# Optimization experiments

Hardware: AMD Instinct MI355X
Metric: run time of the kernel (lower is better)

The kernel has to match this reference:

```python
import jax, jax.numpy as jnp
import numpy as np

B, S, H = 2, 1024, 2048
E, K, I = 32, 4, 512   # num_experts, top_k, moe_intermediate
IS = 512               # shared_expert_intermediate


def setup_inputs() -> dict:
    key = jax.random.key(0)
    ks = jax.random.split(key, 10)
    s = 0.02
    return {
        "hidden_states": jax.random.normal(ks[0], (B, S, H), jnp.float32),
        "Wr": jax.random.normal(ks[1], (E, H), jnp.float32) * s,      # router gate
        "Wg": jax.random.normal(ks[2], (E, I, H), jnp.float32) * s,   # expert gate_proj
        "Wu": jax.random.normal(ks[3], (E, I, H), jnp.float32) * s,   # expert up_proj
        "Wd": jax.random.normal(ks[4], (E, H, I), jnp.float32) * s,   # expert down_proj
        "Wsg": jax.random.normal(ks[5], (IS, H), jnp.float32) * s,    # shared gate_proj
        "Wsu": jax.random.normal(ks[6], (IS, H), jnp.float32) * s,    # shared up_proj
        "Wsd": jax.random.normal(ks[7], (H, IS), jnp.float32) * s,    # shared down_proj
        "Wsgate": jax.random.normal(ks[8], (1, H), jnp.float32) * s,  # shared_expert_gate
    }


def reference(hidden_states, Wr, Wg, Wu, Wd, Wsg, Wsu, Wsd, Wsgate):
    b, s, h = hidden_states.shape
    x = hidden_states.reshape(-1, h)                      # [T, H]
    T = x.shape[0]

    # router: softmax in fp32, top-k, renormalize (norm_topk_prob=True)
    router_logits = x @ Wr.T                               # [T, E]
    rw = jax.nn.softmax(router_logits.astype(jnp.float32), axis=-1)
    vals, idx = jax.lax.top_k(rw, K)                       # [T, K]
    vals = vals / jnp.sum(vals, axis=-1, keepdims=True)
    vals = vals.astype(x.dtype)

    # combine-weight matrix: zeros except selected experts
    C = jnp.zeros((T, E), x.dtype).at[jnp.arange(T)[:, None], idx].add(vals)

    # all experts evaluate all tokens (calibrate_all_experts path); combine zeros non-selected
    g = jnp.einsum('th,eih->tei', x, Wg)                   # [T, E, I]
    u = jnp.einsum('th,eih->tei', x, Wu)
    hact = jax.nn.silu(g) * u
    moe_out = jnp.einsum('tei,ehi,te->th', hact, Wd, C)    # weighted combine

    # shared expert with sigmoid gate
    shared = (jax.nn.silu(x @ Wsg.T) * (x @ Wsu.T)) @ Wsd.T
    gate = jax.nn.sigmoid(x @ Wsgate.T)                    # [T, 1]
    out = (moe_out + gate * shared).reshape(b, s, h)
    return out, router_logits
```

## Files before the change

kernel.cpp:

```cpp
#include <hip/hip_runtime.h>
#include <math.h>

#define T_N 2048
#define H_N 2048
#define E_N 32
#define I_N 512
#define NA_MOE (T_N*4)
#define NA_ALL (NA_MOE + T_N)
#define BM 128
#define BK 32
#define MAXT 112

typedef short s16x8 __attribute__((ext_vector_type(8)));
typedef float f32x4 __attribute__((ext_vector_type(4)));

__device__ inline short f2bf(float f){
    unsigned int u = __float_as_uint(f);
    u = (u + 0x7fffu + ((u >> 16) & 1u)) >> 16;
    return (short)u;
}
__device__ inline float bf2f(short s){
    return __uint_as_float(((unsigned int)(unsigned short)s) << 16);
}
__device__ inline s16x8 cvt8(float4 f0, float4 f1){
    s16x8 v;
    v[0]=f2bf(f0.x); v[1]=f2bf(f0.y); v[2]=f2bf(f0.z); v[3]=f2bf(f0.w);
    v[4]=f2bf(f1.x); v[5]=f2bf(f1.y); v[6]=f2bf(f1.z); v[7]=f2bf(f1.w);
    return v;
}

__global__ __launch_bounds__(256) void cast_x_kernel(const float* __restrict__ x,
                                                     short* __restrict__ xbf){
    size_t i = (size_t)(blockIdx.x * 256 + threadIdx.x) * 8;
    float4 a = *(const float4*)(x + i);
    float4 b = *(const float4*)(x + i + 4);
    *(s16x8*)(xbf + i) = cvt8(a, b);
}

__global__ __launch_bounds__(64) void router_kernel(
    const float* __restrict__ x, const float* __restrict__ Wr,
    const float* __restrict__ Wsgate,
    float* __restrict__ logits_out, int* __restrict__ tidx, float* __restrict__ tw,
    int* __restrict__ perm, float* __restrict__ wgt, int* __restrict__ counts)
{
    const int t = blockIdx.x, lane = threadIdx.x;
    const float* xr = x + (size_t)t * H_N;
    float xv[32];
    #pragma unroll
    for (int i = 0; i < 32; i++) xv[i] = xr[i*64 + lane];
    __shared__ float lg[34];
    for (int e = 0; e < 33; e++){
        const float* wr = (e < 32) ? (Wr + (size_t)e * H_N) : Wsgate;
        double s = 0.0;
        #pragma unroll
        for (int i = 0; i < 32; i++) s += (double)xv[i] * (double)wr[i*64 + lane];
        #pragma unroll
        for (int o = 32; o > 0; o >>= 1) s += __shfl_down(s, o);
        if (lane == 0) lg[e] = (float)s;
    }
    __syncthreads();
    if (lane < 32) logits_out[(size_t)t*32 + lane] = lg[lane];
    if (lane == 0){
        float m = lg[0];
        for (int e = 1; e < 32; e++) m = fmaxf(m, lg[e]);
        unsigned mask = 0; int sel[4]; float sv[4]; float s4 = 0.f;
        for (int k = 0; k < 4; k++){
            int best = -1; float bv = -1e30f;
            for (int e = 0; e < 32; e++)
                if (!((mask >> e) & 1u) && lg[e] > bv){ bv = lg[e]; best = e; }
            mask |= 1u << best; sel[k] = best;
            float p = expf(lg[best] - m); sv[k] = p; s4 += p;
        }
        for (int k = 0; k < 4; k++){
            tidx[t*4 + k] = sel[k];
            tw[t*4 + k]   = sv[k] / s4;
            atomicAdd(&counts[sel[k]], 1);
        }
        perm[NA_MOE + t] = t;
        wgt[NA_MOE + t]  = 1.f / (1.f + expf(-lg[32]));
    }
}

__global__ void scan_kernel(int* ctrl){
    if (threadIdx.x == 0){
        int* counts = ctrl; int* eoff = ctrl + 128; int* ecnt = ctrl + 192;
        int acc = 0;
        for (int e = 0; e < 32; e++){ eoff[e] = acc; ecnt[e] = counts[e]; acc += counts[e]; }
        eoff[32] = NA_MOE; ecnt[32] = T_N;
        int nt = 0;
        for (int e = 0; e < 33; e++){
            int c = ecnt[e];
            for (int m = 0; m * BM < c; m++) ctrl[260 + nt++] = (e << 16) | m;
        }
        ctrl[256] = nt;
    }
    if (threadIdx.x < 64) ctrl[64 + threadIdx.x] = 0;
}

__global__ __launch_bounds__(256) void scatter_kernel(
    const int* __restrict__ tidx, const float* __restrict__ tw,
    int* __restrict__ perm, float* __restrict__ wgt, int* __restrict__ apos,
    int* ctrl)
{
    int t = blockIdx.x * 256 + threadIdx.x;
    if (t >= T_N) return;
    const int* eoff = ctrl + 128; int* cursor = ctrl + 64;
    for (int k = 0; k < 4; k++){
        int e = tidx[t*4 + k];
        int pos = eoff[e] + atomicAdd(&cursor[e], 1);
        perm[pos] = t; wgt[pos] = tw[t*4 + k]; apos[t*4 + k] = pos;
    }
}

__global__ __launch_bounds__(256, 3) void gemm1_kernel(
    const short* __restrict__ xbf,
    const float* __restrict__ Wg, const float* __restrict__ Wu,
    const float* __restrict__ Wsg, const float* __restrict__ Wsu,
    const int* __restrict__ perm, const int* __restrict__ ctrl,
    short* __restrict__ hact)
{
    const int tile = blockIdx.x >> 3;
    if (tile >= ctrl[256]) return;
    const int wrk = ctrl[260 + tile];
    const int e   = wrk >> 16;
    const int m0  = (wrk & 0xffff) << 7;
    const int cnt = ctrl[192 + e];
    const int off = ctrl[128 + e];
    const int n0  = (blockIdx.x & 7) << 6;

    __shared__ s16x8 lsA[2][4*128];
    __shared__ s16x8 lsBg[2][4*64];
    __shared__ s16x8 lsBu[2][4*64];

    const int tid = threadIdx.x;
    const int r_a = tid & 127;
    const int kca = tid >> 7;
    const short* arow = nullptr;
    if (m0 + r_a < cnt) arow = xbf + (size_t)perm[off + m0 + r_a] * H_N;

    const int rb = tid >> 2, kcb = tid & 3;
    const float *browg, *browu;
    if (e < 32){
        browg = Wg + ((size_t)e * I_N + (n0 + rb)) * H_N + kcb*8;
        browu = Wu + ((size_t)e * I_N + (n0 + rb)) * H_N + kcb*8;
    } else {
        browg = Wsg + (size_t)(n0 + rb) * H_N + kcb*8;
        browu = Wsu + (size_t)(n0 + rb) * H_N + kcb*8;
    }

    const int wid = tid >> 6, lane = tid & 63;
    const int wm = wid >> 1, wn = wid & 1;
    const int kg = lane >> 4, l15 = lane & 15;

    f32x4 accg[4][2], accu[4][2];
    #pragma unroll
    for (int a = 0; a < 4; a++)
        #pragma unroll
        for (int b = 0; b < 2; b++)
            #pragma unroll
            for (int j = 0; j < 4; j++){ accg[a][b][j] = 0.f; accu[a][b][j] = 0.f; }

    {
        s16x8 a0{}, a1{};
        if (arow){
            a0 = *(const s16x8*)(arow + kca*8);
            a1 = *(const s16x8*)(arow + (kca+2)*8);
        }
        lsA[0][kca*128 + r_a]     = a0;
        lsA[0][(kca+2)*128 + r_a] = a1;
        float4 g0 = *(const float4*)(browg);
        float4 g1 = *(const float4*)(browg + 4);
        float4 u0 = *(const float4*)(browu);
        float4 u1 = *(const float4*)(browu + 4);
        lsBg[0][kcb*64 + rb] = cvt8(g0, g1);
        lsBu[0][kcb*64 + rb] = cvt8(u0, u1);
    }
    s16x8 pa0{}, pa1{};
    if (arow){
        pa0 = *(const s16x8*)(arow + BK + kca*8);
        pa1 = *(const s16x8*)(arow + BK + (kca+2)*8);
    }
    float4 pg0 = *(const float4*)(browg + BK);
    float4 pg1 = *(const float4*)(browg + BK + 4);
    float4 pu0 = *(const float4*)(browu + BK);
    float4 pu1 = *(const float4*)(browu + BK + 4);

    int cur = 0;
    for (int k0 = 0; k0 < H_N; k0 += BK){
        __syncthreads();
        s16x8 na0{}, na1{};
        float4 ng0{}, ng1{}, nu0{}, nu1{};
        if (k0 + 2*BK < H_N){
            const int kn = k0 + 2*BK;
            if (arow){
                na0 = *(const s16x8*)(arow + kn + kca*8);
                na1 = *(const s16x8*)(arow + kn + (kca+2)*8);
            }
            ng0 = *(const float4*)(browg + kn);
            ng1 = *(const float4*)(browg + kn + 4);
            nu0 = *(const float4*)(browu + kn);
            nu1 = *(const float4*)(browu + kn + 4);
        }
        if (k0 + BK < H_N){
            const int nb = cur ^ 1;
            lsA[nb][kca*128 + r_a]     = pa0;
            lsA[nb][(kca+2)*128 + r_a] = pa1;
            lsBg[nb][kcb*64 + rb] = cvt8(pg0, pg1);
            lsBu[nb][kcb*64 + rb] = cvt8(pu0, pu1);
        }
        #pragma unroll
        for (int mf = 0; mf < 4; mf++){
            s16x8 a = lsA[cur][kg*128 + wm*64 + mf*16 + l15];
            #pragma unroll
            for (int nf = 0; nf < 2; nf++){
                s16x8 bg = lsBg[cur][kg*64 + wn*32 + nf*16 + l15];
                s16x8 bu = lsBu[cur][kg*64 + wn*32 + nf*16 + l15];
                accg[mf][nf] = __builtin_amdgcn_mfma_f32_16x16x32_bf16(a, bg, accg[mf][nf], 0, 0, 0);
                accu[mf][nf] = __builtin_amdgcn_mfma_f32_16x16x32_bf16(a, bu, accu[mf][nf], 0, 0, 0);
            }
        }
        pa0 = na0; pa1 = na1;
        pg0 = ng0; pg1 = ng1; pu0 = nu0; pu1 = nu1;
        cur ^= 1;
    }
    #pragma unroll
    for (int mf = 0; mf < 4; mf++){
        #pragma unroll
        for (int j = 0; j < 4; j++){
            int row = m0 + wm*64 + mf*16 + kg*4 + j;
            if (row < cnt){
                #pragma unroll
                for (int nf = 0; nf < 2; nf++){
                    int col = n0 + wn*32 + nf*16 + l15;
                    float g = accg[mf][nf][j], u = accu[mf][nf][j];
                    float h = g / (1.f + expf(-g)) * u;
                    hact[(size_t)(off + row) * I_N + col] = f2bf(h);
                }
            }
        }
    }
}

template<int USE_Y>
__global__ __launch_bounds__(256, 3) void gemm2_kernel(
    const short* __restrict__ hact,
    const float* __restrict__ Wd, const float* __restrict__ Wsd,
    const int* __restrict__ perm, const float* __restrict__ wgt,
    const int* __restrict__ ctrl, float* __restrict__ out, short* __restrict__ y)
{
    const int tile = blockIdx.x >> 5;
    if (tile >= ctrl[256]) return;
    const int wrk = ctrl[260 + tile];
    const int e   = wrk >> 16;
    const int m0  = (wrk & 0xffff) << 7;
    const int cnt = ctrl[192 + e];
    const int off = ctrl[128 + e];
    const int n0  = (blockIdx.x & 31) << 6;

    __shared__ s16x8 lsA[2][4*128];
    __shared__ s16x8 lsB[2][4*64];

    const int tid = threadIdx.x;
    const int r_a = tid & 127;
    const int kca = tid >> 7;
    const short* arow = nullptr;
    if (m0 + r_a < cnt) arow = hact + (size_t)(off + m0 + r_a) * I_N;

    const int rb = tid >> 2, kcb = tid & 3;
    const float* brow = (e < 32) ? (Wd  + ((size_t)e * H_N + (n0 + rb)) * I_N + kcb*8)
                                 : (Wsd + (size_t)(n0 + rb) * I_N + kcb*8);

    const int wid = tid >> 6, lane = tid & 63;
    const int wm = wid >> 1, wn = wid & 1;
    const int kg = lane >> 4, l15 = lane & 15;

    f32x4 acc[4][2];
    #pragma unroll
    for (int a = 0; a < 4; a++)
        #pragma unroll
        for (int b = 0; b < 2; b++)
            #pragma unroll
            for (int j = 0; j < 4; j++) acc[a][b][j] = 0.f;

    {
        s16x8 a0{}, a1{};
        if (arow){
            a0 = *(const s16x8*)(arow + kca*8);
            a1 = *(const s16x8*)(arow + (kca+2)*8);
        }
        lsA[0][kca*128 + r_a]     = a0;
        lsA[0][(kca+2)*128 + r_a] = a1;
        float4 f0 = *(const float4*)(brow);
        float4 f1 = *(const float4*)(brow + 4);
        lsB[0][kcb*64 + rb] = cvt8(f0, f1);
    }
    s16x8 pa0{}, pa1{};
    if (arow){
        pa0 = *(const s16x8*)(arow + BK + kca*8);
        pa1 = *(const s16x8*)(arow + BK + (kca+2)*8);
    }
    float4 pf0 = *(const float4*)(brow + BK);
    float4 pf1 = *(const float4*)(brow + BK + 4);

    int cur = 0;
    for (int k0 = 0; k0 < I_N; k0 += BK){
        __syncthreads();
        s16x8 na0{}, na1{};
        float4 nf0{}, nf1{};
        if (k0 + 2*BK < I_N){
            const int kn = k0 + 2*BK;
            if (arow){
                na0 = *(const s16x8*)(arow + kn + kca*8);
                na1 = *(const s16x8*)(arow + kn + (kca+2)*8);
            }
            nf0 = *(const float4*)(brow + kn);
            nf1 = *(const float4*)(brow + kn + 4);
        }
        if (k0 + BK < I_N){
            const int nb = cur ^ 1;
            lsA[nb][kca*128 + r_a]     = pa0;
            lsA[nb][(kca+2)*128 + r_a] = pa1;
            lsB[nb][kcb*64 + rb] = cvt8(pf0, pf1);
        }
        #pragma unroll
        for (int mf = 0; mf < 4; mf++){
            s16x8 a = lsA[cur][kg*128 + wm*64 + mf*16 + l15];
            #pragma unroll
            for (int nf = 0; nf < 2; nf++){
                s16x8 b = lsB[cur][kg*64 + wn*32 + nf*16 + l15];
                acc[mf][nf] = __builtin_amdgcn_mfma_f32_16x16x32_bf16(a, b, acc[mf][nf], 0, 0, 0);
            }
        }
        pa0 = na0; pa1 = na1; pf0 = nf0; pf1 = nf1;
        cur ^= 1;
    }
    #pragma unroll
    for (int mf = 0; mf < 4; mf++){
        #pragma unroll
        for (int j = 0; j < 4; j++){
            int row = m0 + wm*64 + mf*16 + kg*4 + j;
            if (row < cnt){
                int aidx = off + row;
                if (USE_Y){
                    #pragma unroll
                    for (int nf = 0; nf < 2; nf++){
                        int col = n0 + wn*32 + nf*16 + l15;
                        y[(size_t)aidx * H_N + col] = f2bf(acc[mf][nf][j]);
                    }
                } else {
                    int tok = perm[aidx];
                    float w = wgt[aidx];
                    #pragma unroll
                    for (int nf = 0; nf < 2; nf++){
                        int col = n0 + wn*32 + nf*16 + l15;
                        atomicAdd(&out[(size_t)tok * H_N + col], w * acc[mf][nf][j]);
                    }
                }
            }
        }
    }
}

__global__ __launch_bounds__(256) void combine_kernel(
    const short* __restrict__ y, const int* __restrict__ apos,
    const float* __restrict__ tw, const float* __restrict__ wgt,
    float* __restrict__ out)
{
    const int t = blockIdx.x;
    const int c0 = threadIdx.x * 8;
    float acc[8];
    {
        float ws = wgt[NA_MOE + t];
        s16x8 v = *(const s16x8*)(y + (size_t)(NA_MOE + t) * H_N + c0);
        #pragma unroll
        for (int j = 0; j < 8; j++) acc[j] = ws * bf2f(v[j]);
    }
    #pragma unroll
    for (int k = 0; k < 4; k++){
        int p   = apos[t*4 + k];
        float w = tw[t*4 + k];
        s16x8 v = *(const s16x8*)(y + (size_t)p * H_N + c0);
        #pragma unroll
        for (int j = 0; j < 8; j++) acc[j] += w * bf2f(v[j]);
    }
    float4 o0 = make_float4(acc[0], acc[1], acc[2], acc[3]);
    float4 o1 = make_float4(acc[4], acc[5], acc[6], acc[7]);
    *(float4*)(out + (size_t)t * H_N + c0)     = o0;
    *(float4*)(out + (size_t)t * H_N + c0 + 4) = o1;
}

extern "C" void kernel_launch(void* const* d_in, const int* in_sizes, int n_in,
                              void* d_out, int out_size, void* d_ws, size_t ws_size,
                              hipStream_t stream)
{
    const float* x      = (const float*)d_in[0];
    const float* Wr     = (const float*)d_in[1];
    const float* Wg     = (const float*)d_in[2];
    const float* Wu     = (const float*)d_in[3];
    const float* Wd     = (const float*)d_in[4];
    const float* Wsg    = (const float*)d_in[5];
    const float* Wsu    = (const float*)d_in[6];
    const float* Wsd    = (const float*)d_in[7];
    const float* Wsgate = (const float*)d_in[8];

    float* out    = (float*)d_out;
    float* logits = out + (size_t)T_N * H_N;

    char* ws = (char*)d_ws;
    short* xbf  = (short*)ws;
    short* hact = (short*)(ws + 8388608);
    int*   perm = (int*)(ws + 18874368);
    float* wgt  = (float*)(ws + 18915328);
    int*   tidx = (int*)(ws + 18956288);
    float* tw   = (float*)(ws + 18989056);
    int*   apos = (int*)(ws + 19021824);
    int*   ctrl = (int*)(ws + 19054592);
    short* y    = (short*)(ws + 19056640);
    const size_t Y_END = 19056640ull + 41943040ull;
    const bool use_y = (ws_size >= Y_END);

    hipMemsetAsync(ctrl, 0, 256 * sizeof(int), stream);
    if (!use_y)
        hipMemsetAsync(d_out, 0, (size_t)T_N * H_N * sizeof(float), stream);

    cast_x_kernel<<<2048, 256, 0, stream>>>(x, xbf);
    router_kernel<<<T_N, 64, 0, stream>>>(x, Wr, Wsgate, logits, tidx, tw, perm, wgt, ctrl);
    scan_kernel<<<1, 64, 0, stream>>>(ctrl);
    scatter_kernel<<<T_N/256, 256, 0, stream>>>(tidx, tw, perm, wgt, apos, ctrl);
    gemm1_kernel<<<MAXT*8, 256, 0, stream>>>(xbf, Wg, Wu, Wsg, Wsu, perm, ctrl, hact);
    if (use_y){
        gemm2_kernel<1><<<MAXT*32, 256, 0, stream>>>(hact, Wd, Wsd, perm, wgt, ctrl, out, y);
        combine_kernel<<<T_N, 256, 0, stream>>>(y, apos, tw, wgt, out);
    } else {
        gemm2_kernel<0><<<MAXT*32, 256, 0, stream>>>(hact, Wd, Wsd, perm, wgt, ctrl, out, y);
    }
}
```

Baseline: 366.6 us.

## Use 256-row tiles, split-K gemm1 with fixup kernel, reorder shared tiles first

Raises the M tile to 256 rows in both grouped GEMMs, so each expert weight tile is reused across more tokens and fewer fp32 weight reads plus bf16 conversions are needed. To keep enough blocks in flight for gemm1, it narrows N to 32 and can split the H reduction in two. The split writes fp32 partials for gate and up, and a new fixup kernel sums them and applies SiLU. The shared-expert tiles are now scheduled first. The split path costs about 80MB of extra partial-sum traffic and one more launch, and only runs when the workspace is large enough.

```diff
diff --git a/kernel.cpp b/kernel.cpp
--- a/kernel.cpp
+++ b/kernel.cpp
@@ -7,9 +7,10 @@
 #define I_N 512
 #define NA_MOE (T_N*4)
 #define NA_ALL (NA_MOE + T_N)
-#define BM 128
+#define BM 256
 #define BK 32
-#define MAXT 112
+#define MAXT 72
+#define PART_FLOATS 10485760ull
 
 typedef short s16x8 __attribute__((ext_vector_type(8)));
 typedef float f32x4 __attribute__((ext_vector_type(4)));
@@ -88,7 +89,8 @@
         for (int e = 0; e < 32; e++){ eoff[e] = acc; ecnt[e] = counts[e]; acc += counts[e]; }
         eoff[32] = NA_MOE; ecnt[32] = T_N;
         int nt = 0;
-        for (int e = 0; e < 33; e++){
+        for (int m = 0; m * BM < T_N; m++) ctrl[260 + nt++] = (32 << 16) | m;
+        for (int e = 0; e < 32; e++){
             int c = ecnt[e];
             for (int m = 0; m * BM < c; m++) ctrl[260 + nt++] = (e << 16) | m;
         }
@@ -112,44 +114,43 @@
     }
 }
 
+template<int KS>
 __global__ __launch_bounds__(256, 3) void gemm1_kernel(
     const short* __restrict__ xbf,
     const float* __restrict__ Wg, const float* __restrict__ Wu,
     const float* __restrict__ Wsg, const float* __restrict__ Wsu,
     const int* __restrict__ perm, const int* __restrict__ ctrl,
-    short* __restrict__ hact)
-{
-    const int tile = blockIdx.x >> 3;
+    short* __restrict__ hact, float* __restrict__ part)
+{
+    const int bid  = blockIdx.x;
+    const int tile = bid / (16*KS);
     if (tile >= ctrl[256]) return;
+    const int sub = bid % (16*KS);
+    const int nb  = (KS==2) ? (sub >> 1) : sub;
+    const int kh  = (KS==2) ? (sub & 1) : 0;
+    const int KH  = H_N / KS;
     const int wrk = ctrl[260 + tile];
     const int e   = wrk >> 16;
-    const int m0  = (wrk & 0xffff) << 7;
+    const int m0  = (wrk & 0xffff) << 8;
     const int cnt = ctrl[192 + e];
     const int off = ctrl[128 + e];
-    const int n0  = (blockIdx.x & 7) << 6;
-
-    __shared__ s16x8 lsA[2][4*128];
-    __shared__ s16x8 lsBg[2][4*64];
-    __shared__ s16x8 lsBu[2][4*64];
+    const int n0  = nb * 32;
+
+    __shared__ s16x8 lsA[2][4*256];
+    __shared__ s16x8 lsBg[2][4*32];
+    __shared__ s16x8 lsBu[2][4*32];
 
     const int tid = threadIdx.x;
-    const int r_a = tid & 127;
-    const int kca = tid >> 7;
     const short* arow = nullptr;
-    if (m0 + r_a < cnt) arow = xbf + (size_t)perm[off + m0 + r_a] * H_N;
-
-    const int rb = tid >> 2, kcb = tid & 3;
-    const float *browg, *browu;
-    if (e < 32){
-        browg = Wg + ((size_t)e * I_N + (n0 + rb)) * H_N + kcb*8;
-        browu = Wu + ((size_t)e * I_N + (n0 + rb)) * H_N + kcb*8;
-    } else {
-        browg = Wsg + (size_t)(n0 + rb) * H_N + kcb*8;
-        browu = Wsu + (size_t)(n0 + rb) * H_N + kcb*8;
-    }
+    if (m0 + tid < cnt) arow = xbf + (size_t)perm[off + m0 + tid] * H_N + kh*KH;
+    const int tb  = tid & 127;
+    const int rb  = tb & 31, kcb = tb >> 5;
+    const float* brow;
+    if (e < 32) brow = ((tid < 128) ? Wg : Wu) + ((size_t)e*I_N + n0 + rb)*H_N + kh*KH + kcb*8;
+    else        brow = ((tid < 128) ? Wsg : Wsu) + (size_t)(n0 + rb)*H_N + kh*KH + kcb*8;
 
     const int wid = tid >> 6, lane = tid & 63;
-    const int wm = wid >> 1, wn = wid & 1;
+    const int wm = wid;
     const int kg = lane >> 4, l15 = lane & 15;
 
     f32x4 accg[4][2], accu[4][2];
@@ -161,84 +162,130 @@
             for (int j = 0; j < 4; j++){ accg[a][b][j] = 0.f; accu[a][b][j] = 0.f; }
 
     {
-        s16x8 a0{}, a1{};
+        s16x8 a[4] = {{0},{0},{0},{0}};
         if (arow){
-            a0 = *(const s16x8*)(arow + kca*8);
-            a1 = *(const s16x8*)(arow + (kca+2)*8);
-        }
-        lsA[0][kca*128 + r_a]     = a0;
-        lsA[0][(kca+2)*128 + r_a] = a1;
-        float4 g0 = *(const float4*)(browg);
-        float4 g1 = *(const float4*)(browg + 4);
-        float4 u0 = *(const float4*)(browu);
-        float4 u1 = *(const float4*)(browu + 4);
-        lsBg[0][kcb*64 + rb] = cvt8(g0, g1);
-        lsBu[0][kcb*64 + rb] = cvt8(u0, u1);
-    }
-    s16x8 pa0{}, pa1{};
+            #pragma unroll
+            for (int kc = 0; kc < 4; kc++) a[kc] = *(const s16x8*)(arow + kc*8);
+        }
+        #pragma unroll
+        for (int kc = 0; kc < 4; kc++) lsA[0][kc*256 + tid] = a[kc];
+        float4 f0 = *(const float4*)(brow);
+        float4 f1 = *(const float4*)(brow + 4);
+        ((tid < 128) ? lsBg[0] : lsBu[0])[kcb*32 + rb] = cvt8(f0, f1);
+    }
+    s16x8 pa[4] = {{0},{0},{0},{0}};
     if (arow){
-        pa0 = *(const s16x8*)(arow + BK + kca*8);
-        pa1 = *(const s16x8*)(arow + BK + (kca+2)*8);
-    }
-    float4 pg0 = *(const float4*)(browg + BK);
-    float4 pg1 = *(const float4*)(browg + BK + 4);
-    float4 pu0 = *(const float4*)(browu + BK);
-    float4 pu1 = *(const float4*)(browu + BK + 4);
+        #pragma unroll
+        for (int kc = 0; kc < 4; kc++) pa[kc] = *(const s16x8*)(arow + BK + kc*8);
+    }
+    float4 pf0 = *(const float4*)(brow + BK);
+    float4 pf1 = *(const float4*)(brow + BK + 4);
 
     int cur = 0;
-    for (int k0 = 0; k0 < H_N; k0 += BK){
+    for (int k0 = 0; k0 < KH; k0 += BK){
         __syncthreads();
-        s16x8 na0{}, na1{};
-        float4 ng0{}, ng1{}, nu0{}, nu1{};
-        if (k0 + 2*BK < H_N){
+        s16x8 na[4] = {{0},{0},{0},{0}};
+        float4 nf0{}, nf1{};
+        if (k0 + 2*BK < KH){
             const int kn = k0 + 2*BK;
             if (arow){
-                na0 = *(const s16x8*)(arow + kn + kca*8);
-                na1 = *(const s16x8*)(arow + kn + (kca+2)*8);
-            }
-            ng0 = *(const float4*)(browg + kn);
-            ng1 = *(const float4*)(browg + kn + 4);
-            nu0 = *(const float4*)(browu + kn);
-            nu1 = *(const float4*)(browu + kn + 4);
-        }
-        if (k0 + BK < H_N){
-            const int nb = cur ^ 1;
-            lsA[nb][kca*128 + r_a]     = pa0;
-            lsA[nb][(kca+2)*128 + r_a] = pa1;
-            lsBg[nb][kcb*64 + rb] = cvt8(pg0, pg1);
-            lsBu[nb][kcb*64 + rb] = cvt8(pu0, pu1);
+                #pragma unroll
+                for (int kc = 0; kc < 4; kc++) na[kc] = *(const s16x8*)(arow + kn + kc*8);
+            }
+            nf0 = *(const float4*)(brow + kn);
+            nf1 = *(const float4*)(brow + kn + 4);
+        }
+        if (k0 + BK < KH){
+            const int nbuf = cur ^ 1;
+            #pragma unroll
+            for (int kc = 0; kc < 4; kc++) lsA[nbuf][kc*256 + tid] = pa[kc];
+            ((tid < 128) ? lsBg[nbuf] : lsBu[nbuf])[kcb*32 + rb] = cvt8(pf0, pf1);
         }
         #pragma unroll
         for (int mf = 0; mf < 4; mf++){
-            s16x8 a = lsA[cur][kg*128 + wm*64 + mf*16 + l15];
+            s16x8 a = lsA[cur][kg*256 + wm*64 + mf*16 + l15];
             #pragma unroll
             for (int nf = 0; nf < 2; nf++){
-                s16x8 bg = lsBg[cur][kg*64 + wn*32 + nf*16 + l15];
-                s16x8 bu = lsBu[cur][kg*64 + wn*32 + nf*16 + l15];
+                s16x8 bg = lsBg[cur][kg*32 + nf*16 + l15];
+                s16x8 bu = lsBu[cur][kg*32 + nf*16 + l15];
                 accg[mf][nf] = __builtin_amdgcn_mfma_f32_16x16x32_bf16(a, bg, accg[mf][nf], 0, 0, 0);
                 accu[mf][nf] = __builtin_amdgcn_mfma_f32_16x16x32_bf16(a, bu, accu[mf][nf], 0, 0, 0);
             }
         }
-        pa0 = na0; pa1 = na1;
-        pg0 = ng0; pg1 = ng1; pu0 = nu0; pu1 = nu1;
+        #pragma unroll
+        for (int kc = 0; kc < 4; kc++) pa[kc] = na[kc];
+        pf0 = nf0; pf1 = nf1;
         cur ^= 1;
     }
-    #pragma unroll
-    for (int mf = 0; mf < 4; mf++){
-        #pragma unroll
-        for (int j = 0; j < 4; j++){
-            int row = m0 + wm*64 + mf*16 + kg*4 + j;
-            if (row < cnt){
-                #pragma unroll
-                for (int nf = 0; nf < 2; nf++){
-                    int col = n0 + wn*32 + nf*16 + l15;
-                    float g = accg[mf][nf][j], u = accu[mf][nf][j];
-                    float h = g / (1.f + expf(-g)) * u;
-                    hact[(size_t)(off + row) * I_N + col] = f2bf(h);
+
+    if (KS == 2){
+        float* pb = part + (size_t)kh * PART_FLOATS;
+        #pragma unroll
+        for (int mf = 0; mf < 4; mf++){
+            #pragma unroll
+            for (int j = 0; j < 4; j++){
+                int row = m0 + wm*64 + mf*16 + kg*4 + j;
+                if (row < cnt){
+                    float* pr = pb + (size_t)(off + row) * 1024 + n0;
+                    #pragma unroll
+                    for (int nf = 0; nf < 2; nf++){
+                        __builtin_nontemporal_store(accg[mf][nf][j], pr + nf*16 + l15);
+                        __builtin_nontemporal_store(accu[mf][nf][j], pr + 512 + nf*16 + l15);
+                    }
                 }
             }
         }
-    }
+    } else {
+        #pragma unroll
+        for (int mf = 0; mf < 4; mf++){
+            #pragma unroll
+            for (int j = 0; j < 4; j++){
+                int row = m0 + wm*64 + mf*16 + kg*4 + j;
+                if (row < cnt){
+                    #pragma unroll
+                    for (int nf = 0; nf < 2; nf++){
+                        int col = n0 + nf*16 + l15;
+                        float g = accg[mf][nf][j], u = accu[mf][nf][j];
+                        float h = g / (1.f + expf(-g)) * u;
+                        hact[(size_t)(off + row) * I_N + col] = f2bf(h);
+                    }
+                }
+            }
+        }
+    }
+}
+
+__global__ __launch_bounds__(256) void fixup_kernel(const float* __restrict__ part,
+                                                    short* __restrict__ hact){
+    size_t base = ((size_t)blockIdx.x * 256 + threadIdx.x) * 8;
+    int row = (int)(base >> 9);
+    int c   = (int)(base & 511);
+    const float* pg0 = part + (size_t)row * 1024 + c;
+    const float* pg1 = pg0 + PART_FLOATS;
+    float g[8], u[8];
+    {
+        f32x4 a0 = __builtin_nontemporal_load((const f32x4*)pg0);
+        f32x4 a1 = __builtin_nontemporal_load((const f32x4*)(pg0 + 4));
+        f32x4 b0 = __builtin_nontemporal_load((const f32x4*)pg1);
+        f32x4 b1 = __builtin_nontemporal_load((const f32x4*)(pg1 + 4));
+        #pragma unroll
+        for (int j = 0; j < 4; j++){ g[j] = a0[j] + b0[j]; g[4+j] = a1[j] + b1[j]; }
+    }
+    {
+        f32x4 a0 = __builtin_nontemporal_load((const f32x4*)(pg0 + 512));
+        f32x4 a1 = __builtin_nontemporal_load((const f32x4*)(pg0 + 516));
+        f32x4 b0 = __builtin_nontemporal_load((const f32x4*)(pg1 + 512));
+        f32x4 b1 = __builtin_nontemporal_load((const f32x4*)(pg1 + 516));
+        #pragma unroll
+        for (int j = 0; j < 4; j++){ u[j] = a0[j] + b0[j]; u[4+j] = a1[j] + b1[j]; }
+    }
+    s16x8 v;
+    #pragma unroll
+    for (int j = 0; j < 8; j++){
+        float h = g[j] / (1.f + expf(-g[j])) * u[j];
+        v[j] = f2bf(h);
+    }
+    *(s16x8*)(hact + (size_t)row * I_N + c) = v;
 }
 
 template<int USE_Y>
@@ -250,54 +297,52 @@
 {
     const int tile = blockIdx.x >> 5;
     if (tile >= ctrl[256]) return;
+    const int nb  = blockIdx.x & 31;
     const int wrk = ctrl[260 + tile];
     const int e   = wrk >> 16;
-    const int m0  = (wrk & 0xffff) << 7;
+    const int m0  = (wrk & 0xffff) << 8;
     const int cnt = ctrl[192 + e];
     const int off = ctrl[128 + e];
-    const int n0  = (blockIdx.x & 31) << 6;
-
-    __shared__ s16x8 lsA[2][4*128];
+    const int n0  = nb * 64;
+
+    __shared__ s16x8 lsA[2][4*256];
     __shared__ s16x8 lsB[2][4*64];
 
     const int tid = threadIdx.x;
-    const int r_a = tid & 127;
-    const int kca = tid >> 7;
     const short* arow = nullptr;
-    if (m0 + r_a < cnt) arow = hact + (size_t)(off + m0 + r_a) * I_N;
-
-    const int rb = tid >> 2, kcb = tid & 3;
-    const float* brow = (e < 32) ? (Wd  + ((size_t)e * H_N + (n0 + rb)) * I_N + kcb*8)
+    if (m0 + tid < cnt) arow = hact + (size_t)(off + m0 + tid) * I_N;
+    const int rb = tid & 63, kcb = tid >> 6;
+    const float* brow = (e < 32) ? (Wd  + ((size_t)e * H_N + n0 + rb) * I_N + kcb*8)
                                  : (Wsd + (size_t)(n0 + rb) * I_N + kcb*8);
 
     const int wid = tid >> 6, lane = tid & 63;
-    const int wm = wid >> 1, wn = wid & 1;
+    const int wm = wid;
     const int kg = lane >> 4, l15 = lane & 15;
 
-    f32x4 acc[4][2];
+    f32x4 acc[4][4];
     #pragma unroll
     for (int a = 0; a < 4; a++)
         #pragma unroll
-        for (int b = 0; b < 2; b++)
+        for (int b = 0; b < 4; b++)
             #pragma unroll
             for (int j = 0; j < 4; j++) acc[a][b][j] = 0.f;
 
     {
-        s16x8 a0{}, a1{};
+        s16x8 a[4] = {{0},{0},{0},{0}};
         if (arow){
-            a0 = *(const s16x8*)(arow + kca*8);
-            a1 = *(const s16x8*)(arow + (kca+2)*8);
-        }
-        lsA[0][kca*128 + r_a]     = a0;
-        lsA[0][(kca+2)*128 + r_a] = a1;
+            #pragma unroll
+            for (int kc = 0; kc < 4; kc++) a[kc] = *(const s16x8*)(arow + kc*8);
+        }
+        #pragma unroll
+        for (int kc = 0; kc < 4; kc++) lsA[0][kc*256 + tid] = a[kc];
         float4 f0 = *(const float4*)(brow);
         float4 f1 = *(const float4*)(brow + 4);
         lsB[0][kcb*64 + rb] = cvt8(f0, f1);
     }
-    s16x8 pa0{}, pa1{};
+    s16x8 pa[4] = {{0},{0},{0},{0}};
     if (arow){
-        pa0 = *(const s16x8*)(arow + BK + kca*8);
-        pa1 = *(const s16x8*)(arow + BK + (kca+2)*8);
+        #pragma unroll
+        for (int kc = 0; kc < 4; kc++) pa[kc] = *(const s16x8*)(arow + BK + kc*8);
     }
     float4 pf0 = *(const float4*)(brow + BK);
     float4 pf1 = *(const float4*)(brow + BK + 4);
@@ -305,33 +350,35 @@
     int cur = 0;
     for (int k0 = 0; k0 < I_N; k0 += BK){
         __syncthreads();
-        s16x8 na0{}, na1{};
+        s16x8 na[4] = {{0},{0},{0},{0}};
         float4 nf0{}, nf1{};
         if (k0 + 2*BK < I_N){
             const int kn = k0 + 2*BK;
             if (arow){
-                na0 = *(const s16x8*)(arow + kn + kca*8);
-                na1 = *(const s16x8*)(arow + kn + (kca+2)*8);
+                #pragma unroll
+                for (int kc = 0; kc < 4; kc++) na[kc] = *(const s16x8*)(arow + kn + kc*8);
             }
             nf0 = *(const float4*)(brow + kn);
             nf1 = *(const float4*)(brow + kn + 4);
         }
         if (k0 + BK < I_N){
-            const int nb = cur ^ 1;
-            lsA[nb][kca*128 + r_a]     = pa0;
-            lsA[nb][(kca+2)*128 + r_a] = pa1;
-            lsB[nb][kcb*64 + rb] = cvt8(pf0, pf1);
+            const int nbuf = cur ^ 1;
+            #pragma unroll
+            for (int kc = 0; kc < 4; kc++) lsA[nbuf][kc*256 + tid] = pa[kc];
+            lsB[nbuf][kcb*64 + rb] = cvt8(pf0, pf1);
         }
         #pragma unroll
         for (int mf = 0; mf < 4; mf++){
-            s16x8 a = lsA[cur][kg*128 + wm*64 + mf*16 + l15];
-            #pragma unroll
-            for (int nf = 0; nf < 2; nf++){
-                s16x8 b = lsB[cur][kg*64 + wn*32 + nf*16 + l15];
+            s16x8 a = lsA[cur][kg*256 + wm*64 + mf*16 + l15];
+            #pragma unroll
+            for (int nf = 0; nf < 4; nf++){
+                s16x8 b = lsB[cur][kg*64 + nf*16 + l15];
                 acc[mf][nf] = __builtin_amdgcn_mfma_f32_16x16x32_bf16(a, b, acc[mf][nf], 0, 0, 0);
             }
         }
-        pa0 = na0; pa1 = na1; pf0 = nf0; pf1 = nf1;
+        #pragma unroll
+        for (int kc = 0; kc < 4; kc++) pa[kc] = na[kc];
+        pf0 = nf0; pf1 = nf1;
         cur ^= 1;
     }
     #pragma unroll
@@ -343,16 +390,16 @@
                 int aidx = off + row;
                 if (USE_Y){
                     #pragma unroll
-                    for (int nf = 0; nf < 2; nf++){
-                        int col = n0 + wn*32 + nf*16 + l15;
+                    for (int nf = 0; nf < 4; nf++){
+                        int col = n0 + nf*16 + l15;
                         y[(size_t)aidx * H_N + col] = f2bf(acc[mf][nf][j]);
                     }
                 } else {
                     int tok = perm[aidx];
                     float w = wgt[aidx];
                     #pragma unroll
-                    for (int nf = 0; nf < 2; nf++){
-                        int col = n0 + wn*32 + nf*16 + l15;
+                    for (int nf = 0; nf < 4; nf++){
+                        int col = n0 + nf*16 + l15;
                         atomicAdd(&out[(size_t)tok * H_N + col], w * acc[mf][nf][j]);
                     }
                 }
@@ -416,8 +463,9 @@
     int*   apos = (int*)(ws + 19021824);
     int*   ctrl = (int*)(ws + 19054592);
     short* y    = (short*)(ws + 19056640);
-    const size_t Y_END = 19056640ull + 41943040ull;
-    const bool use_y = (ws_size >= Y_END);
+    float* part = (float*)(ws + 60999680);
+    const bool use_y    = (ws_size >= 60999680ull);
+    const bool use_part = (ws_size >= 144885760ull);
 
     hipMemsetAsync(ctrl, 0, 256 * sizeof(int), stream);
     if (!use_y)
@@ -427,7 +475,12 @@
     router_kernel<<<T_N, 64, 0, stream>>>(x, Wr, Wsgate, logits, tidx, tw, perm, wgt, ctrl);
     scan_kernel<<<1, 64, 0, stream>>>(ctrl);
     scatter_kernel<<<T_N/256, 256, 0, stream>>>(tidx, tw, perm, wgt, apos, ctrl);
-    gemm1_kernel<<<MAXT*8, 256, 0, stream>>>(xbf, Wg, Wu, Wsg, Wsu, perm, ctrl, hact);
+    if (use_part){
+        gemm1_kernel<2><<<MAXT*32, 256, 0, stream>>>(xbf, Wg, Wu, Wsg, Wsu, perm, ctrl, hact, part);
+        fixup_kernel<<<(NA_ALL*I_N)/(256*8), 256, 0, stream>>>(part, hact);
+    } else {
+        gemm1_kernel<1><<<MAXT*16, 256, 0, stream>>>(xbf, Wg, Wu, Wsg, Wsu, perm, ctrl, hact, part);
+    }
     if (use_y){
         gemm2_kernel<1><<<MAXT*32, 256, 0, stream>>>(hact, Wd, Wsd, perm, wgt, ctrl, out, y);
         combine_kernel<<<T_N, 256, 0, stream>>>(y, apos, tw, wgt, out);
```

After: 476.9 us. +30.1%, slower.

## Load A tiles directly into LDS, use hardware bf16 convert, schedule shared tiles first

Applied to the files above, without the earlier changes.

Both grouped GEMMs now stage their bf16 A-operand tiles with global_load_lds, going straight from global memory to LDS. This replaces the register prefetch and LDS store, and invalid rows are clamped to the last valid row instead of using null-pointer guards. The float-to-bf16 conversion now uses a hardware __bf16 cast instead of manual rounding. The weight-staging thread mapping is reordered so each thread stores to LDS index tid. The scan places the shared-expert tiles first in the work list, presumably to start the largest uniform work early. This removes VGPR pressure and LDS store instructions but relies on the compiler handling async LDS-load waits correctly before barriers.

```diff
diff --git a/kernel.cpp b/kernel.cpp
--- a/kernel.cpp
+++ b/kernel.cpp
@@ -14,10 +14,19 @@
 typedef short s16x8 __attribute__((ext_vector_type(8)));
 typedef float f32x4 __attribute__((ext_vector_type(4)));
 
+typedef __attribute__((address_space(1))) unsigned int gu32;
+typedef __attribute__((address_space(3))) unsigned int lu32;
+
+__device__ inline void gload16(const void* g, void* l){
+#if __has_builtin(__builtin_amdgcn_global_load_lds)
+    __builtin_amdgcn_global_load_lds((gu32*)g, (lu32*)l, 16, 0, 0);
+#else
+    *(s16x8*)l = *(const s16x8*)g;
+#endif
+}
+
 __device__ inline short f2bf(float f){
-    unsigned int u = __float_as_uint(f);
-    u = (u + 0x7fffu + ((u >> 16) & 1u)) >> 16;
-    return (short)u;
+    return __builtin_bit_cast(short, (__bf16)f);
 }
 __device__ inline float bf2f(short s){
     return __uint_as_float(((unsigned int)(unsigned short)s) << 16);
@@ -88,7 +97,8 @@
         for (int e = 0; e < 32; e++){ eoff[e] = acc; ecnt[e] = counts[e]; acc += counts[e]; }
         eoff[32] = NA_MOE; ecnt[32] = T_N;
         int nt = 0;
-        for (int e = 0; e < 33; e++){
+        for (int m = 0; m * BM < T_N; m++) ctrl[260 + nt++] = (32 << 16) | m;
+        for (int e = 0; e < 32; e++){
             int c = ecnt[e];
             for (int m = 0; m * BM < c; m++) ctrl[260 + nt++] = (e << 16) | m;
         }
@@ -135,10 +145,10 @@
     const int tid = threadIdx.x;
     const int r_a = tid & 127;
     const int kca = tid >> 7;
-    const short* arow = nullptr;
-    if (m0 + r_a < cnt) arow = xbf + (size_t)perm[off + m0 + r_a] * H_N;
-
-    const int rb = tid >> 2, kcb = tid & 3;
+    int srow = off + ((m0 + r_a < cnt) ? (m0 + r_a) : (cnt - 1));
+    const short* arow = xbf + (size_t)perm[srow] * H_N;
+
+    const int rb = tid & 63, kcb = tid >> 6;
     const float *browg, *browu;
     if (e < 32){
         browg = Wg + ((size_t)e * I_N + (n0 + rb)) * H_N + kcb*8;
@@ -160,25 +170,15 @@
             #pragma unroll
             for (int j = 0; j < 4; j++){ accg[a][b][j] = 0.f; accu[a][b][j] = 0.f; }
 
+    gload16(arow + kca*8,        &lsA[0][kca*128 + r_a]);
+    gload16(arow + (kca+2)*8,    &lsA[0][(kca+2)*128 + r_a]);
     {
-        s16x8 a0{}, a1{};
-        if (arow){
-            a0 = *(const s16x8*)(arow + kca*8);
-            a1 = *(const s16x8*)(arow + (kca+2)*8);
-        }
-        lsA[0][kca*128 + r_a]     = a0;
-        lsA[0][(kca+2)*128 + r_a] = a1;
         float4 g0 = *(const float4*)(browg);
         float4 g1 = *(const float4*)(browg + 4);
         float4 u0 = *(const float4*)(browu);
         float4 u1 = *(const float4*)(browu + 4);
-        lsBg[0][kcb*64 + rb] = cvt8(g0, g1);
-        lsBu[0][kcb*64 + rb] = cvt8(u0, u1);
-    }
-    s16x8 pa0{}, pa1{};
-    if (arow){
-        pa0 = *(const s16x8*)(arow + BK + kca*8);
-        pa1 = *(const s16x8*)(arow + BK + (kca+2)*8);
+        lsBg[0][tid] = cvt8(g0, g1);
+        lsBu[0][tid] = cvt8(u0, u1);
     }
     float4 pg0 = *(const float4*)(browg + BK);
     float4 pg1 = *(const float4*)(browg + BK + 4);
@@ -188,25 +188,19 @@
     int cur = 0;
     for (int k0 = 0; k0 < H_N; k0 += BK){
         __syncthreads();
-        s16x8 na0{}, na1{};
-        float4 ng0{}, ng1{}, nu0{}, nu1{};
+        const int nbuf = cur ^ 1;
+        if (k0 + BK < H_N){
+            gload16(arow + k0 + BK + kca*8,     &lsA[nbuf][kca*128 + r_a]);
+            gload16(arow + k0 + BK + (kca+2)*8, &lsA[nbuf][(kca+2)*128 + r_a]);
+            lsBg[nbuf][tid] = cvt8(pg0, pg1);
+            lsBu[nbuf][tid] = cvt8(pu0, pu1);
+        }
         if (k0 + 2*BK < H_N){
             const int kn = k0 + 2*BK;
-            if (arow){
-                na0 = *(const s16x8*)(arow + kn + kca*8);
-                na1 = *(const s16x8*)(arow + kn + (kca+2)*8);
-            }
-            ng0 = *(const float4*)(browg + kn);
-            ng1 = *(const float4*)(browg + kn + 4);
-            nu0 = *(const float4*)(browu + kn);
-            nu1 = *(const float4*)(browu + kn + 4);
-        }
-        if (k0 + BK < H_N){
-            const int nb = cur ^ 1;
-            lsA[nb][kca*128 + r_a]     = pa0;
-            lsA[nb][(kca+2)*128 + r_a] = pa1;
-            lsBg[nb][kcb*64 + rb] = cvt8(pg0, pg1);
-            lsBu[nb][kcb*64 + rb] = cvt8(pu0, pu1);
+            pg0 = *(const float4*)(browg + kn);
+            pg1 = *(const float4*)(browg + kn + 4);
+            pu0 = *(const float4*)(browu + kn);
+            pu1 = *(const float4*)(browu + kn + 4);
         }
         #pragma unroll
         for (int mf = 0; mf < 4; mf++){
@@ -219,8 +213,6 @@
                 accu[mf][nf] = __builtin_amdgcn_mfma_f32_16x16x32_bf16(a, bu, accu[mf][nf], 0, 0, 0);
             }
         }
-        pa0 = na0; pa1 = na1;
-        pg0 = ng0; pg1 = ng1; pu0 = nu0; pu1 = nu1;
         cur ^= 1;
     }
     #pragma unroll
@@ -263,11 +255,11 @@
     const int tid = threadIdx.x;
     const int r_a = tid & 127;
     const int kca = tid >> 7;
-    const short* arow = nullptr;
-    if (m0 + r_a < cnt) arow = hact + (size_t)(off + m0 + r_a) * I_N;
-
-    const int rb = tid >> 2, kcb = tid & 3;
-    const float* brow = (e < 32) ? (Wd  + ((size_t)e * H_N + (n0 + rb)) * I_N + kcb*8)
+    int srow = off + ((m0 + r_a < cnt) ? (m0 + r_a) : (cnt - 1));
+    const short* arow = hact + (size_t)srow * I_N;
+
+    const int rb = tid & 63, kcb = tid >> 6;
+    const float* brow = (e < 32) ? (Wd  + ((size_t)e * H_N + n0 + rb) * I_N + kcb*8)
                                  : (Wsd + (size_t)(n0 + rb) * I_N + kcb*8);
 
     const int wid = tid >> 6, lane = tid & 63;
@@ -282,22 +274,12 @@
             #pragma unroll
             for (int j = 0; j < 4; j++) acc[a][b][j] = 0.f;
 
+    gload16(arow + kca*8,     &lsA[0][kca*128 + r_a]);
+    gload16(arow + (kca+2)*8, &lsA[0][(kca+2)*128 + r_a]);
     {
-        s16x8 a0{}, a1{};
-        if (arow){
-            a0 = *(const s16x8*)(arow + kca*8);
-            a1 = *(const s16x8*)(arow + (kca+2)*8);
-        }
-        lsA[0][kca*128 + r_a]     = a0;
-        lsA[0][(kca+2)*128 + r_a] = a1;
         float4 f0 = *(const float4*)(brow);
         float4 f1 = *(const float4*)(brow + 4);
-        lsB[0][kcb*64 + rb] = cvt8(f0, f1);
-    }
-    s16x8 pa0{}, pa1{};
-    if (arow){
-        pa0 = *(const s16x8*)(arow + BK + kca*8);
-        pa1 = *(const s16x8*)(arow + BK + (kca+2)*8);
+        lsB[0][tid] = cvt8(f0, f1);
     }
     float4 pf0 = *(const float4*)(brow + BK);
     float4 pf1 = *(const float4*)(brow + BK + 4);
@@ -305,22 +287,16 @@
     int cur = 0;
     for (int k0 = 0; k0 < I_N; k0 += BK){
         __syncthreads();
-        s16x8 na0{}, na1{};
-        float4 nf0{}, nf1{};
+        const int nbuf = cur ^ 1;
+        if (k0 + BK < I_N){
+            gload16(arow + k0 + BK + kca*8,     &lsA[nbuf][kca*128 + r_a]);
+            gload16(arow + k0 + BK + (kca+2)*8, &lsA[nbuf][(kca+2)*128 + r_a]);
+            lsB[nbuf][tid] = cvt8(pf0, pf1);
+        }
         if (k0 + 2*BK < I_N){
             const int kn = k0 + 2*BK;
-            if (arow){
-                na0 = *(const s16x8*)(arow + kn + kca*8);
-                na1 = *(const s16x8*)(arow + kn + (kca+2)*8);
-            }
-            nf0 = *(const float4*)(brow + kn);
-            nf1 = *(const float4*)(brow + kn + 4);
-        }
-        if (k0 + BK < I_N){
-            const int nb = cur ^ 1;
-            lsA[nb][kca*128 + r_a]     = pa0;
-            lsA[nb][(kca+2)*128 + r_a] = pa1;
-            lsB[nb][kcb*64 + rb] = cvt8(pf0, pf1);
+            pf0 = *(const float4*)(brow + kn);
+            pf1 = *(const float4*)(brow + kn + 4);
         }
         #pragma unroll
         for (int mf = 0; mf < 4; mf++){
@@ -331,7 +307,6 @@
                 acc[mf][nf] = __builtin_amdgcn_mfma_f32_16x16x32_bf16(a, b, acc[mf][nf], 0, 0, 0);
             }
         }
-        pa0 = na0; pa1 = na1; pf0 = nf0; pf1 = nf1;
         cur ^= 1;
     }
     #pragma unroll
@@ -416,8 +391,7 @@
     int*   apos = (int*)(ws + 19021824);
     int*   ctrl = (int*)(ws + 19054592);
     short* y    = (short*)(ws + 19056640);
-    const size_t Y_END = 19056640ull + 41943040ull;
-    const bool use_y = (ws_size >= Y_END);
+    const bool use_y = (ws_size >= 60999680ull);
 
     hipMemsetAsync(ctrl, 0, 256 * sizeof(int), stream);
     if (!use_y)
```

Measured after the change: 455.9 us. 1.24x slower.
